# Kernel tuning notes

Hardware: AMD Instinct MI355X
Metric: run time of the kernel (lower is better)

## Reference

```python
import jax, jax.numpy as jnp
import numpy as np

H = 32      # n_heads
KV = 8      # n_kv_heads
HD = 64     # head_dim = dim // n_heads


def setup_inputs() -> dict:
    key = jax.random.key(0)
    ks = jax.random.split(key, 8)
    B, S, D = 4, 1024, 2048
    x = jax.random.normal(ks[0], (B, S, D), dtype=jnp.float32)
    # RoPE tables stored as cos/sin parts of the complex freqs_cis (seqlen, head_dim//2)
    pos = jnp.arange(S, dtype=jnp.float32)[:, None]
    inv = 1.0 / (10000.0 ** (jnp.arange(0, HD, 2, dtype=jnp.float32) / HD))[None, :]
    ang = pos * inv                          # (S, HD//2)
    freqs_cos = jnp.cos(ang)
    freqs_sin = jnp.sin(ang)
    # additive causal mask (S, S): 0 on/below diagonal, -inf above
    mask = jnp.where(jnp.tril(jnp.ones((S, S), dtype=bool)), 0.0, -jnp.inf).astype(jnp.float32)
    sc = 0.02
    wq = jax.random.normal(ks[1], (H * HD, D), dtype=jnp.float32) * sc
    wk = jax.random.normal(ks[2], (KV * HD, D), dtype=jnp.float32) * sc
    wv = jax.random.normal(ks[3], (KV * HD, D), dtype=jnp.float32) * sc
    wo = jax.random.normal(ks[4], (D, D), dtype=jnp.float32) * sc
    return {"x": x, "freqs_cos": freqs_cos, "freqs_sin": freqs_sin, "mask": mask,
            "wq": wq, "wk": wk, "wv": wv, "wo": wo}


def _rope(t, cos, sin):
    # t: (B, S, nh, HD). Faithful to source: rotation is indexed by x.shape[2]
    # (the HEAD axis, due to pre-transpose call), broadcast over sequence.
    nh = t.shape[2]
    c = cos[:nh][None, None, :, :]           # (1,1,nh,HD//2)
    s = sin[:nh][None, None, :, :]
    tr = t.reshape(*t.shape[:-1], HD // 2, 2)
    t0, t1 = tr[..., 0], tr[..., 1]
    o0 = t0 * c - t1 * s
    o1 = t0 * s + t1 * c
    return jnp.stack([o0, o1], axis=-1).reshape(t.shape)


def reference(x, freqs_cos, freqs_sin, mask, wq, wk, wv, wo):
    B, S, D = x.shape
    xq = (x @ wq.T).reshape(B, S, H, HD)
    xk = (x @ wk.T).reshape(B, S, KV, HD)
    xv = (x @ wv.T).reshape(B, S, KV, HD)
    xq = _rope(xq, freqs_cos, freqs_sin)
    xk = _rope(xk, freqs_cos, freqs_sin)
    rep = H // KV
    xk = jnp.repeat(xk, rep, axis=2)         # GQA repeat_interleave on head axis
    xv = jnp.repeat(xv, rep, axis=2)
    q = xq.transpose(0, 2, 1, 3)             # (B,H,S,HD)
    k = xk.transpose(0, 2, 1, 3)
    v = xv.transpose(0, 2, 1, 3)
    scores = jnp.einsum('bhqd,bhkd->bhqk', q, k) / np.sqrt(HD).astype(np.float32)
    scores = scores + mask[None, None, :, :]
    p = jax.nn.softmax(scores.astype(jnp.float32), axis=-1).astype(q.dtype)
    out = jnp.einsum('bhqk,bhkd->bhqd', p, v)
    out = out.transpose(0, 2, 1, 3).reshape(B, S, H * HD)
    return out @ wo.T
```

## Files before the change

### kernel.cpp

```cpp
#include <hip/hip_runtime.h>
#include <hip/hip_bf16.h>

constexpr int kB  = 4;
constexpr int kS  = 1024;
constexpr int kD  = 2048;
constexpr int kH  = 32;
constexpr int kKV = 8;
constexpr int kHD = 64;
constexpr int kM  = kB * kS;
constexpr int kNT = kS / 64;

constexpr float kNegBig = -30000.0f;
constexpr float kC = 0.125f * 1.44269504f;
constexpr float kDeferThr = 40.0f;

typedef __attribute__((ext_vector_type(8))) short short8;
typedef __attribute__((ext_vector_type(4))) float floatx4;

static __device__ __forceinline__ short f2bf(float f) {
    unsigned int u = __builtin_bit_cast(unsigned int, f);
    unsigned int lsb = (u >> 16) & 1u;
    u += 0x7fffu + lsb;
    return (short)(u >> 16);
}
static __device__ __forceinline__ short f2bf_fast(float f) {
    unsigned int u = __builtin_bit_cast(unsigned int, f);
    return (short)((u + 0x8000u) >> 16);
}

static __device__ __forceinline__ void load_lds16(const short* g, short* l) {
    __builtin_amdgcn_global_load_lds(
        (const __attribute__((address_space(1))) unsigned int*)g,
        (__attribute__((address_space(3))) unsigned int*)l, 16, 0, 0);
}

__global__ void cast_f2b(const float* __restrict__ in, short* __restrict__ outp, int n4) {
    int gid = blockIdx.x * blockDim.x + threadIdx.x;
    if (gid >= n4) return;
    float4 v = ((const float4*)in)[gid];
    short4 o;
    o.x = f2bf(v.x); o.y = f2bf(v.y); o.z = f2bf(v.z); o.w = f2bf(v.w);
    ((short4*)outp)[gid] = o;
}

__global__ void cast4_f2b(const float* __restrict__ a, const float* __restrict__ b,
                          const float* __restrict__ c, const float* __restrict__ d,
                          short* __restrict__ oa, short* __restrict__ ob,
                          short* __restrict__ oc, short* __restrict__ od,
                          int na4, int nb4, int nc4, int nd4) {
    int gid = blockIdx.x * blockDim.x + threadIdx.x;
    const float* src; short* dst; int idx;
    if (gid < na4)                    { src = a; dst = oa; idx = gid; }
    else if (gid < na4 + nb4)         { src = b; dst = ob; idx = gid - na4; }
    else if (gid < na4 + nb4 + nc4)   { src = c; dst = oc; idx = gid - na4 - nb4; }
    else if (gid < na4+nb4+nc4+nd4)   { src = d; dst = od; idx = gid - na4 - nb4 - nc4; }
    else return;
    float4 v = ((const float4*)src)[idx];
    short4 o;
    o.x = f2bf(v.x); o.y = f2bf(v.y); o.z = f2bf(v.z); o.w = f2bf(v.w);
    ((short4*)dst)[idx] = o;
}

template <typename OT, int ROPE>
__global__ __launch_bounds__(256) void gemm_bt_lds(const short* __restrict__ A,
                                                   const short* __restrict__ Bm,
                                                   OT* __restrict__ C,
                                                   int M, int N, int K,
                                                   const float* __restrict__ cosb,
                                                   const float* __restrict__ sinb,
                                                   short* __restrict__ Vt,
                                                   const short* __restrict__ B2,
                                                   short* __restrict__ Kout) {
    __shared__ short As[128 * 64];
    __shared__ short Bs[128 * 64];

    int tid  = threadIdx.x;
    int wave = tid >> 6, lane = tid & 63;
    int quad = lane >> 4, l16 = lane & 15;
    int wm = wave >> 1, wn = wave & 1;

    int nwg  = gridDim.x * gridDim.y;
    int orig = blockIdx.y * gridDim.x + blockIdx.x;
    int wg   = orig;
    if ((nwg & 7) == 0) {
        int cpx = nwg >> 3;
        wg = (orig & 7) * cpx + (orig >> 3);
    }
    int bx = wg % gridDim.x, by = wg / gridDim.x;
    int m0 = by * 128, n0 = bx * 128;

    const short* Bblk;
    if constexpr (ROPE == 3)
        Bblk = (n0 < 2048) ? Bm + (long)n0 * K : B2 + (long)(n0 - 2048) * K;
    else
        Bblk = Bm + (long)n0 * K;

    floatx4 acc[4][4];
    for (int i = 0; i < 4; i++)
        for (int j = 0; j < 4; j++) acc[i][j] = (floatx4){0.f, 0.f, 0.f, 0.f};

    int srow8 = lane >> 3;
    int scol  = (((lane & 7) ^ srow8) << 3);
    int rsw   = (l16 & 7) << 3;

    for (int k0 = 0; k0 < K; k0 += 64) {
        __syncthreads();
#pragma unroll
        for (int i = 0; i < 4; i++) {
            int r8 = wave * 32 + i * 8;
            load_lds16(A + (long)(m0 + r8 + srow8) * K + k0 + scol, &As[r8 * 64]);
            load_lds16(Bblk + (long)(r8 + srow8) * K + k0 + scol, &Bs[r8 * 64]);
        }
        __syncthreads();

#pragma unroll
        for (int kk = 0; kk < 2; kk++) {
            int rcol = (kk * 32 + quad * 8) ^ rsw;
            short8 af[4], bfr[4];
#pragma unroll
            for (int i = 0; i < 4; i++)
                af[i] = *(const short8*)&As[(wm * 64 + i * 16 + l16) * 64 + rcol];
#pragma unroll
            for (int j = 0; j < 4; j++)
                bfr[j] = *(const short8*)&Bs[(wn * 64 + j * 16 + l16) * 64 + rcol];
#pragma unroll
            for (int i = 0; i < 4; i++)
#pragma unroll
                for (int j = 0; j < 4; j++)
                    acc[i][j] = __builtin_amdgcn_mfma_f32_16x16x32_bf16(
                        af[i], bfr[j], acc[i][j], 0, 0, 0);
        }
    }

    if constexpr (ROPE == 3) {
        for (int j = 0; j < 4; j++) {
            int col = n0 + wn * 64 + j * 16 + l16;
            if (col >= 2560) {
                int cv = col - 2560;
                for (int i = 0; i < 4; i++) {
                    int row0 = m0 + wm * 64 + i * 16 + quad * 4;
                    short4 o;
                    o.x = f2bf(acc[i][j][0]);
                    o.y = f2bf(acc[i][j][1]);
                    o.z = f2bf(acc[i][j][2]);
                    o.w = f2bf(acc[i][j][3]);
                    *(short4*)&Vt[(long)cv * M + row0] = o;
                }
            } else {
                bool isK = col >= 2048;
                int hh = isK ? ((col - 2048) >> 6) : (col >> 6);
                int ii = (col & 63) >> 1;
                float c = cosb[hh * 32 + ii];
                float s = sinb[hh * 32 + ii];
                for (int i = 0; i < 4; i++) {
                    for (int r = 0; r < 4; r++) {
                        int row = m0 + wm * 64 + i * 16 + quad * 4 + r;
                        float v = acc[i][j][r];
                        float p = __shfl_xor(v, 1);
                        v = (col & 1) ? (p * s + v * c)
                                      : (v * c - p * s);
                        if (isK)
                            Kout[(long)row * 1024 + (col - 2048)] = f2bf(v);
                        else
                            ((short*)C)[(long)row * 2048 + col] = f2bf(v);
                    }
                }
            }
        }
    } else {
        for (int j = 0; j < 4; j++) {
            int col = n0 + wn * 64 + j * 16 + l16;
            for (int i = 0; i < 4; i++)
                for (int r = 0; r < 4; r++) {
                    int row = m0 + wm * 64 + i * 16 + quad * 4 + r;
                    float v = acc[i][j][r];
                    if constexpr (sizeof(OT) == 2)
                        C[(long)row * N + col] = f2bf(v);
                    else
                        C[(long)row * N + col] = v;
                }
        }
    }
}

__global__ __launch_bounds__(256) void attn_kernel(const short* __restrict__ xq,
                                                   const short* __restrict__ xk,
                                                   const short* __restrict__ vt,
                                                   short* __restrict__ out,
                                                   int kvstride) {
    __shared__ short pT[4][32][72];

    int pb = blockIdx.x;
    int h = blockIdx.y, b = blockIdx.z;
    int kvh = h >> 2;
    int tid = threadIdx.x, wave = tid >> 6, lane = tid & 63;
    int quad = lane >> 4, l16 = lane & 15;

    const short* kbase0 = xk + (long)b * kS * kvstride + kvh * kHD;
    const short* vbase = vt + (long)kvh * kHD * kM + (long)b * kS;

    short8 ones;
    for (int i = 0; i < 8; i++) ones[i] = (short)0x3F80;

    auto loadK = [&](short8 (&kf)[4][2], int kt) {
        const short* kbase = kbase0 + (long)kt * 64 * kvstride;
#pragma unroll
        for (int kb = 0; kb < 4; kb++) {
            const short* kp = kbase + (long)(kb * 16 + l16) * kvstride + quad * 8;
            kf[kb][0] = *(const short8*)kp;
            kf[kb][1] = *(const short8*)(kp + 32);
        }
    };

    auto process = [&](int c) {
        int r0 = c * 128 + wave * 32;
        int nt = (r0 + 31) / 64 + 1;

        short8 qf[2][2];
#pragma unroll
        for (int g = 0; g < 2; g++) {
            const short* qp = xq + (((long)b * kS + r0 + g * 16 + l16) * kH + h) * kHD + quad * 8;
            qf[g][0] = *(const short8*)(qp);
            qf[g][1] = *(const short8*)(qp + 32);
        }

        float m_run[2][4];
        floatx4 acc_l[2];
        floatx4 acc_o[2][4];
#pragma unroll
        for (int g = 0; g < 2; g++) {
            acc_l[g] = (floatx4){0.f, 0.f, 0.f, 0.f};
            for (int r = 0; r < 4; r++) m_run[g][r] = kNegBig;
            for (int nb = 0; nb < 4; nb++) acc_o[g][nb] = (floatx4){0.f, 0.f, 0.f, 0.f};
        }

        short8 kf[4][2];
        loadK(kf, 0);

        for (int kt = 0; kt < nt; kt++) {
            short8 vf[4][2];
#pragma unroll
            for (int nb = 0; nb < 4; nb++) {
                const short* vp = vbase + (long)(nb * 16 + l16) * kM + kt * 64 + quad * 8;
                vf[nb][0] = *(const short8*)(vp);
                vf[nb][1] = *(const short8*)(vp + 32);
            }

            floatx4 accs[2][4];
            __builtin_amdgcn_s_setprio(1);
#pragma unroll
            for (int g = 0; g < 2; g++)
#pragma unroll
                for (int kb = 0; kb < 4; kb++) {
                    accs[g][kb] = (floatx4){0.f, 0.f, 0.f, 0.f};
                    accs[g][kb] = __builtin_amdgcn_mfma_f32_16x16x32_bf16(qf[g][0], kf[kb][0], accs[g][kb], 0, 0, 0);
                    accs[g][kb] = __builtin_amdgcn_mfma_f32_16x16x32_bf16(qf[g][1], kf[kb][1], accs[g][kb], 0, 0, 0);
                }
            __builtin_amdgcn_s_setprio(0);

            if (kt + 1 < nt) loadK(kf, kt + 1);

#pragma unroll
            for (int g = 0; g < 2; g++) {
                int wr0g = r0 + g * 16;
                if (kt * 64 + 63 > wr0g) {
                    int crow = wr0g + quad * 4;
#pragma unroll
                    for (int kb = 0; kb < 4; kb++)
#pragma unroll
                        for (int r = 0; r < 4; r++) {
                            int kj = kt * 64 + kb * 16 + l16;
                            if (kj > crow + r) accs[g][kb][r] = kNegBig;
                        }
                }
            }

#pragma unroll
            for (int g = 0; g < 2; g++) {
                float mx[4];
#pragma unroll
                for (int r = 0; r < 4; r++) {
                    float m1 = fmaxf(fmaxf(accs[g][0][r], accs[g][1][r]),
                                     fmaxf(accs[g][2][r], accs[g][3][r]));
                    for (int off = 1; off < 16; off <<= 1) m1 = fmaxf(m1, __shfl_xor(m1, off));
                    mx[r] = m1;
                }
                bool small = (mx[0] - m_run[g][0] <= kDeferThr) && (mx[1] - m_run[g][1] <= kDeferThr) &&
                             (mx[2] - m_run[g][2] <= kDeferThr) && (mx[3] - m_run[g][3] <= kDeferThr);
                if (!__all(small)) {
#pragma unroll
                    for (int r = 0; r < 4; r++) {
                        float mnew = fmaxf(m_run[g][r], mx[r]);
                        float alpha = exp2f((m_run[g][r] - mnew) * kC);
                        m_run[g][r] = mnew;
                        acc_l[g][r] *= alpha;
                        for (int nb = 0; nb < 4; nb++) acc_o[g][nb][r] *= alpha;
                    }
                }
#pragma unroll
                for (int r = 0; r < 4; r++) {
                    float mk = m_run[g][r] * kC;
                    for (int kb = 0; kb < 4; kb++)
                        accs[g][kb][r] = exp2f(fmaf(accs[g][kb][r], kC, -mk));
                }
            }

#pragma unroll
            for (int g = 0; g < 2; g++)
#pragma unroll
                for (int r = 0; r < 4; r++)
#pragma unroll
                    for (int kb = 0; kb < 4; kb++)
                        pT[wave][g * 16 + quad * 4 + r][kb * 16 + l16] = f2bf_fast(accs[g][kb][r]);

            __builtin_amdgcn_s_setprio(1);
#pragma unroll
            for (int g = 0; g < 2; g++) {
                short8 pf0 = *(const short8*)&pT[wave][g * 16 + l16][quad * 8];
                short8 pf1 = *(const short8*)&pT[wave][g * 16 + l16][32 + quad * 8];
                acc_l[g] = __builtin_amdgcn_mfma_f32_16x16x32_bf16(pf0, ones, acc_l[g], 0, 0, 0);
                acc_l[g] = __builtin_amdgcn_mfma_f32_16x16x32_bf16(pf1, ones, acc_l[g], 0, 0, 0);
#pragma unroll
                for (int nb = 0; nb < 4; nb++) {
                    acc_o[g][nb] = __builtin_amdgcn_mfma_f32_16x16x32_bf16(pf0, vf[nb][0], acc_o[g][nb], 0, 0, 0);
                    acc_o[g][nb] = __builtin_amdgcn_mfma_f32_16x16x32_bf16(pf1, vf[nb][1], acc_o[g][nb], 0, 0, 0);
                }
            }
            __builtin_amdgcn_s_setprio(0);
        }

#pragma unroll
        for (int g = 0; g < 2; g++)
#pragma unroll
            for (int r = 0; r < 4; r++) {
                float inv = 1.0f / fmaxf(acc_l[g][r], 1e-20f);
                int row = r0 + g * 16 + quad * 4 + r;
                for (int nb = 0; nb < 4; nb++)
                    out[(((long)b * kS + row) * kH + h) * kHD + nb * 16 + l16] =
                        f2bf(acc_o[g][nb][r] * inv);
            }
    };

    process(7 - pb);
    process(pb);
}

extern "C" void kernel_launch(void* const* d_in, const int* in_sizes, int n_in,
                              void* d_out, int out_size, void* d_ws, size_t ws_size,
                              hipStream_t stream) {
    const float* x  = (const float*)d_in[0];
    const float* fc = (const float*)d_in[1];
    const float* fs = (const float*)d_in[2];
    const float* wq = (const float*)d_in[4];
    const float* wk = (const float*)d_in[5];
    const float* wv = (const float*)d_in[6];
    const float* wo = (const float*)d_in[7];

    const int M = kM;
    const long MB = 1l << 20;

    char* ws = (char*)d_ws;
    short* xb   = (short*)(ws);
    short* wqb  = (short*)(ws + 16 * MB);
    short* ao   = (short*)(ws);
    short* wob  = (short*)(ws + 16 * MB);
    char*  dob  = (char*)d_out;
    short* xq   = (short*)(dob);
    short* xkv  = (short*)(dob + 16 * MB);
    short* vt   = (short*)(dob + 24 * MB);
    short* wkvb = (short*)(dob + 28 * MB);

    const int nX  = M * kD;
    const int nWq = kD * kD;
    const int nWk = kKV * kHD * kD;

    int total4 = (nX + nWq + 2 * nWk) / 4;
    cast4_f2b<<<(total4 + 255) / 256, 256, 0, stream>>>(
        x, wq, wk, wv, xb, wqb, wkvb, wkvb + nWk,
        nX / 4, nWq / 4, nWk / 4, nWk / 4);

    gemm_bt_lds<short, 3><<<dim3(3072 / 128, M / 128), 256, 0, stream>>>(
        xb, wqb, xq, M, 3072, kD, fc, fs, vt, wkvb, xkv);

    attn_kernel<<<dim3(4, kH, kB), 256, 0, stream>>>(
        xq, xkv, vt, ao, 1024);

    cast_f2b<<<(nWq / 4 + 255) / 256, 256, 0, stream>>>(wo, wob, nWq / 4);
    gemm_bt_lds<float, 0><<<dim3(kD / 128, M / 128), 256, 0, stream>>>(
        ao, wob, (float*)d_out, M, kD, kD, nullptr, nullptr, nullptr, nullptr, nullptr);
}
```

Baseline: 343.6 us.

## Fuse wo fp32-to-bf16 cast into output projection GEMM B-tile loads

Drops the separate cast kernel for wo. The output GEMM now reads fp32 wo directly, converts it to bf16 in registers and stores it into the swizzled LDS tile. It also raises wave priority around the MFMA block with s_setprio. The fused path saves one launch and a write plus read of the bf16 wo, but each GEMM tile re-reads and re-converts fp32 B (32 M-tiles), doubling the B bytes per tile and moving from async LDS loads to synchronous global loads.

```diff
diff --git a/kernel.cpp b/kernel.cpp
--- a/kernel.cpp
+++ b/kernel.cpp
@@ -61,7 +61,7 @@
     ((short4*)dst)[idx] = o;
 }
 
-template <typename OT, int ROPE>
+template <typename OT, int ROPE, int CASTB>
 __global__ __launch_bounds__(256) void gemm_bt_lds(const short* __restrict__ A,
                                                    const short* __restrict__ Bm,
                                                    OT* __restrict__ C,
@@ -70,7 +70,8 @@
                                                    const float* __restrict__ sinb,
                                                    short* __restrict__ Vt,
                                                    const short* __restrict__ B2,
-                                                   short* __restrict__ Kout) {
+                                                   short* __restrict__ Kout,
+                                                   const float* __restrict__ Bf) {
     __shared__ short As[128 * 64];
     __shared__ short Bs[128 * 64];
 
@@ -89,10 +90,10 @@
     int bx = wg % gridDim.x, by = wg / gridDim.x;
     int m0 = by * 128, n0 = bx * 128;
 
-    const short* Bblk;
+    const short* Bblk = nullptr;
     if constexpr (ROPE == 3)
         Bblk = (n0 < 2048) ? Bm + (long)n0 * K : B2 + (long)(n0 - 2048) * K;
-    else
+    else if constexpr (CASTB == 0)
         Bblk = Bm + (long)n0 * K;
 
     floatx4 acc[4][4];
@@ -109,7 +110,19 @@
         for (int i = 0; i < 4; i++) {
             int r8 = wave * 32 + i * 8;
             load_lds16(A + (long)(m0 + r8 + srow8) * K + k0 + scol, &As[r8 * 64]);
-            load_lds16(Bblk + (long)(r8 + srow8) * K + k0 + scol, &Bs[r8 * 64]);
+            if constexpr (CASTB == 1) {
+                const float* src = Bf + (long)(n0 + r8 + srow8) * K + k0 + scol;
+                float4 v0 = *(const float4*)(src);
+                float4 v1 = *(const float4*)(src + 4);
+                short8 o;
+                o[0] = f2bf(v0.x); o[1] = f2bf(v0.y);
+                o[2] = f2bf(v0.z); o[3] = f2bf(v0.w);
+                o[4] = f2bf(v1.x); o[5] = f2bf(v1.y);
+                o[6] = f2bf(v1.z); o[7] = f2bf(v1.w);
+                *(short8*)&Bs[r8 * 64 + lane * 8] = o;
+            } else {
+                load_lds16(Bblk + (long)(r8 + srow8) * K + k0 + scol, &Bs[r8 * 64]);
+            }
         }
         __syncthreads();
 
@@ -123,12 +136,14 @@
 #pragma unroll
             for (int j = 0; j < 4; j++)
                 bfr[j] = *(const short8*)&Bs[(wn * 64 + j * 16 + l16) * 64 + rcol];
+            __builtin_amdgcn_s_setprio(1);
 #pragma unroll
             for (int i = 0; i < 4; i++)
 #pragma unroll
                 for (int j = 0; j < 4; j++)
                     acc[i][j] = __builtin_amdgcn_mfma_f32_16x16x32_bf16(
                         af[i], bfr[j], acc[i][j], 0, 0, 0);
+            __builtin_amdgcn_s_setprio(0);
         }
     }
 
@@ -363,7 +378,6 @@
     short* xb   = (short*)(ws);
     short* wqb  = (short*)(ws + 16 * MB);
     short* ao   = (short*)(ws);
-    short* wob  = (short*)(ws + 16 * MB);
     char*  dob  = (char*)d_out;
     short* xq   = (short*)(dob);
     short* xkv  = (short*)(dob + 16 * MB);
@@ -379,13 +393,13 @@
         x, wq, wk, wv, xb, wqb, wkvb, wkvb + nWk,
         nX / 4, nWq / 4, nWk / 4, nWk / 4);
 
-    gemm_bt_lds<short, 3><<<dim3(3072 / 128, M / 128), 256, 0, stream>>>(
-        xb, wqb, xq, M, 3072, kD, fc, fs, vt, wkvb, xkv);
+    gemm_bt_lds<short, 3, 0><<<dim3(3072 / 128, M / 128), 256, 0, stream>>>(
+        xb, wqb, xq, M, 3072, kD, fc, fs, vt, wkvb, xkv, nullptr);
 
     attn_kernel<<<dim3(4, kH, kB), 256, 0, stream>>>(
         xq, xkv, vt, ao, 1024);
 
-    cast_f2b<<<(nWq / 4 + 255) / 256, 256, 0, stream>>>(wo, wob, nWq / 4);
-    gemm_bt_lds<float, 0><<<dim3(kD / 128, M / 128), 256, 0, stream>>>(
-        ao, wob, (float*)d_out, M, kD, kD, nullptr, nullptr, nullptr, nullptr, nullptr);
-}
+    gemm_bt_lds<float, 0, 1><<<dim3(kD / 128, M / 128), 256, 0, stream>>>(
+        ao, nullptr, (float*)d_out, M, kD, kD, nullptr, nullptr,
+        nullptr, nullptr, nullptr, wo);
+}
```

Measured after the change: 363.8 us. 1.06x slower.
